# Optimization experiments

Hardware: AMD Instinct MI355X
Metric: run time of the kernel (lower is better)

## Reference

```python
import jax, jax.numpy as jnp
import numpy as np

EPS = 0.1  # FAConv default eps


def setup_inputs() -> dict:
    key = jax.random.key(0)
    k1, k2, k3, k4, k5 = jax.random.split(key, 5)
    N, D, E, Dout = 50000, 128, 600000, 128
    x = jax.random.normal(k1, (N, D), dtype=jnp.float32)
    edge_index = jax.random.randint(k2, (2, E), 0, N, dtype=jnp.int64)
    # glorot-style scale for att vectors (Linear(D,1)) and weight matrix
    att_l = jax.random.normal(k3, (D,), dtype=jnp.float32) * (1.0 / np.sqrt(D))
    att_r = jax.random.normal(k4, (D,), dtype=jnp.float32) * (1.0 / np.sqrt(D))
    weight = jax.random.normal(k5, (D, Dout), dtype=jnp.float32) * np.sqrt(6.0 / (D + Dout))
    bias = jnp.zeros((Dout,), dtype=jnp.float32)
    return {"x": x, "edge_index": edge_index, "att_l": att_l, "att_r": att_r,
            "weight": weight, "bias": bias}


def reference(x, edge_index, att_l, att_r, weight, bias):
    N, D = x.shape
    # gcn_norm with add_self_loops=True
    loops = jnp.arange(N, dtype=edge_index.dtype)
    row = jnp.concatenate([edge_index[0], loops])  # source nodes
    col = jnp.concatenate([edge_index[1], loops])  # target nodes
    deg = jax.ops.segment_sum(jnp.ones_like(col, dtype=x.dtype), col, num_segments=N)
    dinv = jnp.where(deg > 0, jax.lax.rsqrt(jnp.maximum(deg, 1e-12)), 0.0)
    norm = dinv[row] * dinv[col]  # [E+N]
    # FAConv attention: alpha = tanh(att_l . x_j + att_r . x_i)
    al = x @ att_l  # [N]
    ar = x @ att_r  # [N]
    a = jnp.tanh(al[row] + ar[col])  # per-edge
    msg = x[row] * (a * norm)[:, None]  # [E+N, D]
    agg = jax.ops.segment_sum(msg, col, num_segments=N)
    h = agg + EPS * x  # x_0 == x in SAGNN.forward
    return h @ weight + bias
```

## Files before the change

kernel.cpp:

```cpp
#include <hip/hip_runtime.h>
#include <hip/hip_bf16.h>

#define FA_EPS 0.1f
#define BUCKET_M 48

typedef _Float16 half8  __attribute__((ext_vector_type(8)));
typedef _Float16 half4v __attribute__((ext_vector_type(4)));
typedef float    f32x4  __attribute__((ext_vector_type(4)));

__device__ __forceinline__ float fast_tanh(float x) {
    float z = __builtin_amdgcn_exp2f(x * 2.885390081777927f);
    return 1.f - 2.f * __builtin_amdgcn_rcpf(z + 1.f);
}


__global__ __launch_bounds__(256) void k_node_prep(
    const float* __restrict__ x,
    const float* __restrict__ att_l,
    const float* __restrict__ att_r,
    const float* __restrict__ w,
    uint2* __restrict__ R, float* __restrict__ ar,
    _Float16* __restrict__ x16, _Float16* __restrict__ wt, int N)
{
    int gtid = (int)(blockIdx.x * blockDim.x + threadIdx.x);
    if (gtid < 128 * 128) {
        int k = gtid >> 7, n = gtid & 127;
        wt[n * 128 + k] = (_Float16)w[k * 128 + n];
    }
    int wave = gtid >> 6;
    int lane = threadIdx.x & 63;
    int half = lane >> 5;
    int sl   = lane & 31;
    int node = wave * 2 + half;
    if (node >= N) return;
    const float4* xr = (const float4*)(x + (size_t)node * 128);
    float4 v  = xr[sl];
    float4 l4 = ((const float4*)att_l)[sl];
    float4 r4 = ((const float4*)att_r)[sl];
    half4v hv;
    hv[0] = (_Float16)v.x; hv[1] = (_Float16)v.y;
    hv[2] = (_Float16)v.z; hv[3] = (_Float16)v.w;
    *((half4v*)(x16 + (size_t)node * 128) + sl) = hv;
    float pal = v.x * l4.x + v.y * l4.y + v.z * l4.z + v.w * l4.w;
    float par = v.x * r4.x + v.y * r4.y + v.z * r4.z + v.w * r4.w;
    #pragma unroll
    for (int off = 16; off > 0; off >>= 1) {
        pal += __shfl_xor(pal, off);
        par += __shfl_xor(par, off);
    }
    if (sl == 0) {
        R[node] = make_uint2(0u, __float_as_uint(pal));
        ar[node] = par;
    }
}

__global__ __launch_bounds__(256) void k_edge(
    const int* __restrict__ ei,
    uint2* __restrict__ R,
    unsigned int* __restrict__ csr, int E)
{
    int e = (int)(blockIdx.x * blockDim.x + threadIdx.x);
    if (e >= E) return;
    int s = ei[e];
    int t = ei[E + e];
    unsigned int pos = atomicAdd((unsigned int*)(R + t), 1u);
    if (pos < BUCKET_M)
        csr[(size_t)t * BUCKET_M + pos] = (unsigned int)s;
}

__global__ __launch_bounds__(256) void k_gather(
    const _Float16* __restrict__ x16,
    const unsigned int* __restrict__ csr,
    const uint2* __restrict__ R,
    const float* __restrict__ ar,
    _Float16* __restrict__ h16, int N)
{
    int wave = (int)((blockIdx.x * blockDim.x + threadIdx.x) >> 6);
    int lane = threadIdx.x & 63;
    int g  = lane >> 4;
    int sl = lane & 15;
    int t  = wave * 4 + g;
    bool valid = t < N;
    int tc = valid ? t : N - 1;
    uint2 rt = R[tc];
    unsigned int dt = rt.x;
    float al_t = __uint_as_float(rt.y);
    float ar_t = ar[tc];
    unsigned int cnt = dt < BUCKET_M ? dt : BUCKET_M;
    if (!valid) cnt = 0u;
    float dinv_t = __builtin_amdgcn_rsqf((float)(dt + 1u));
    const unsigned int* cs = csr + (size_t)tc * BUCKET_M;
    float acc[8];
    #pragma unroll
    for (int c = 0; c < 8; ++c) acc[c] = 0.f;
    int gbase = lane & 0x30;
    for (unsigned int j0 = 0; j0 < cnt; j0 += 16) {
        unsigned int nb = cnt - j0; if (nb > 16u) nb = 16u;
        unsigned int myidx = j0 + (unsigned int)sl;
        bool own = myidx < cnt;
        unsigned int em = cs[own ? myidx : cnt - 1u];
        uint2 rsm = R[em];
        float am = own ? fast_tanh(__uint_as_float(rsm.y) + ar_t)
                         * __builtin_amdgcn_rsqf((float)(rsm.x + 1u))
                       : 0.f;
        const uint4* bp = (const uint4*)(cs + j0);
        uint4 b0 = bp[0], b1 = bp[1], b2 = bp[2], b3 = bp[3];
        unsigned int eu[16];
        eu[0]=b0.x;  eu[1]=b0.y;  eu[2]=b0.z;  eu[3]=b0.w;
        eu[4]=b1.x;  eu[5]=b1.y;  eu[6]=b1.z;  eu[7]=b1.w;
        eu[8]=b2.x;  eu[9]=b2.y;  eu[10]=b2.z; eu[11]=b2.w;
        eu[12]=b3.x; eu[13]=b3.y; eu[14]=b3.z; eu[15]=b3.w;
        half8 v[16];
        #pragma unroll
        for (int u = 0; u < 16; ++u) {
            unsigned int e = (u < (int)nb) ? eu[u] : 0u;
            v[u] = *((const half8*)(x16 + (size_t)e * 128) + sl);
        }
        #pragma unroll
        for (int u = 0; u < 16; ++u) {
            float a = __shfl(am, gbase + u);
            #pragma unroll
            for (int c = 0; c < 8; ++c) acc[c] += a * (float)v[u][c];
        }
    }
    float selfc = fast_tanh(al_t + ar_t) * dinv_t * dinv_t + FA_EPS;
    half8 vt = *((const half8*)(x16 + (size_t)tc * 128) + sl);
    #pragma unroll
    for (int c = 0; c < 8; ++c) acc[c] = acc[c] * dinv_t + selfc * (float)vt[c];
    if (valid) {
        half8 hv;
        #pragma unroll
        for (int c = 0; c < 8; ++c) hv[c] = (_Float16)acc[c];
        *((half8*)(h16 + (size_t)t * 128) + sl) = hv;
    }
}

__global__ __launch_bounds__(256) void k_matmul_mfma(
    const _Float16* __restrict__ h16,
    const _Float16* __restrict__ wt,
    const float* __restrict__ bias,
    float* __restrict__ out, int N)
{
    __shared__ _Float16 wl[128 * 136];
    int tid = threadIdx.x;
    {
        const float* wsrc = (const float*)wt;
        float* wdst = (float*)wl;
        #pragma unroll
        for (int i = tid; i < 8192; i += 256)
            wdst[(i >> 6) * 68 + (i & 63)] = wsrc[i];
    }
    __syncthreads();
    int wv   = tid >> 6;
    int lane = tid & 63;
    int m    = lane & 15;
    int quad = lane >> 4;
    int r0 = (int)blockIdx.x * 64 + wv * 16;
    f32x4 acc[8];
    #pragma unroll
    for (int t = 0; t < 8; ++t) acc[t] = (f32x4)0.f;
    const _Float16* arow = h16 + (size_t)(r0 + m) * 128 + quad * 8;
    #pragma unroll
    for (int k0 = 0; k0 < 128; k0 += 32) {
        half8 a = *(const half8*)(arow + k0);
        #pragma unroll
        for (int t = 0; t < 8; ++t) {
            const _Float16* bp = wl + (size_t)(t * 16 + m) * 136 + quad * 8 + k0;
            half8 b = *(const half8*)bp;
            acc[t] = __builtin_amdgcn_mfma_f32_16x16x32_f16(a, b, acc[t], 0, 0, 0);
        }
    }
    int orow = r0 + quad * 4;
    #pragma unroll
    for (int t = 0; t < 8; ++t) {
        int col = t * 16 + m;
        float bc = bias[col];
        #pragma unroll
        for (int rg = 0; rg < 4; ++rg) {
            int r = orow + rg;
            if (r < N) out[(size_t)r * 128 + col] = acc[t][rg] + bc;
        }
    }
}

extern "C" void kernel_launch(void* const* d_in, const int* in_sizes, int n_in,
                              void* d_out, int out_size, void* d_ws, size_t ws_size,
                              hipStream_t stream)
{
    const float* x     = (const float*)d_in[0];
    const int*   ei    = (const int*)d_in[1];
    const float* att_l = (const float*)d_in[2];
    const float* att_r = (const float*)d_in[3];
    const float* w     = (const float*)d_in[4];
    const float* bias  = (const float*)d_in[5];
    float* out = (float*)d_out;

    const int N  = in_sizes[0] / 128;
    const int E  = in_sizes[1] / 2;
    const int NP = ((N + 63) / 64) * 64;

    char* ws = (char*)d_ws;
    _Float16*     h16 = (_Float16*)ws;
    _Float16*     x16 = h16 + (size_t)NP * 128;
    uint2*        R   = (uint2*)(x16 + (size_t)N * 128);
    float*        ar  = (float*)(R + N);
    unsigned int* csr = (unsigned int*)(ar + N);
    _Float16*     wt  = (_Float16*)(csr + (size_t)N * BUCKET_M);

    {
        int waves = (N + 1) / 2;
        k_node_prep<<<(waves * 64 + 255) / 256, 256, 0, stream>>>(
            x, att_l, att_r, w, R, ar, x16, wt, N);
    }
    k_edge<<<(E + 255) / 256, 256, 0, stream>>>(ei, R, csr, E);
    {
        int waves = (N + 3) / 4;
        k_gather<<<(waves * 64 + 255) / 256, 256, 0, stream>>>(
            x16, csr, R, ar, h16, N);
    }
    k_matmul_mfma<<<NP / 64, 256, 0, stream>>>(h16, wt, bias, out, N);
}
```

Before: 156.6 us.

## Fuse neighbor gather into MFMA matmul via shared-memory staging of h

Merges the gather/aggregation kernel and the MFMA matmul kernel into one. Each block aggregates 64 target rows into an LDS tile, then multiplies that tile by the LDS-resident weight. This removes the fp16 h round trip through global memory and one kernel launch. In exchange it uses more LDS per block and has fewer independent waves per row chunk, which may lower occupancy and the latency hiding of the random gathers.

```diff
diff --git a/kernel.cpp b/kernel.cpp
--- a/kernel.cpp
+++ b/kernel.cpp
@@ -68,80 +68,17 @@
         csr[(size_t)t * BUCKET_M + pos] = (unsigned int)s;
 }
 
-__global__ __launch_bounds__(256) void k_gather(
+__global__ __launch_bounds__(256) void k_gather_mm(
     const _Float16* __restrict__ x16,
     const unsigned int* __restrict__ csr,
     const uint2* __restrict__ R,
     const float* __restrict__ ar,
-    _Float16* __restrict__ h16, int N)
-{
-    int wave = (int)((blockIdx.x * blockDim.x + threadIdx.x) >> 6);
-    int lane = threadIdx.x & 63;
-    int g  = lane >> 4;
-    int sl = lane & 15;
-    int t  = wave * 4 + g;
-    bool valid = t < N;
-    int tc = valid ? t : N - 1;
-    uint2 rt = R[tc];
-    unsigned int dt = rt.x;
-    float al_t = __uint_as_float(rt.y);
-    float ar_t = ar[tc];
-    unsigned int cnt = dt < BUCKET_M ? dt : BUCKET_M;
-    if (!valid) cnt = 0u;
-    float dinv_t = __builtin_amdgcn_rsqf((float)(dt + 1u));
-    const unsigned int* cs = csr + (size_t)tc * BUCKET_M;
-    float acc[8];
-    #pragma unroll
-    for (int c = 0; c < 8; ++c) acc[c] = 0.f;
-    int gbase = lane & 0x30;
-    for (unsigned int j0 = 0; j0 < cnt; j0 += 16) {
-        unsigned int nb = cnt - j0; if (nb > 16u) nb = 16u;
-        unsigned int myidx = j0 + (unsigned int)sl;
-        bool own = myidx < cnt;
-        unsigned int em = cs[own ? myidx : cnt - 1u];
-        uint2 rsm = R[em];
-        float am = own ? fast_tanh(__uint_as_float(rsm.y) + ar_t)
-                         * __builtin_amdgcn_rsqf((float)(rsm.x + 1u))
-                       : 0.f;
-        const uint4* bp = (const uint4*)(cs + j0);
-        uint4 b0 = bp[0], b1 = bp[1], b2 = bp[2], b3 = bp[3];
-        unsigned int eu[16];
-        eu[0]=b0.x;  eu[1]=b0.y;  eu[2]=b0.z;  eu[3]=b0.w;
-        eu[4]=b1.x;  eu[5]=b1.y;  eu[6]=b1.z;  eu[7]=b1.w;
-        eu[8]=b2.x;  eu[9]=b2.y;  eu[10]=b2.z; eu[11]=b2.w;
-        eu[12]=b3.x; eu[13]=b3.y; eu[14]=b3.z; eu[15]=b3.w;
-        half8 v[16];
-        #pragma unroll
-        for (int u = 0; u < 16; ++u) {
-            unsigned int e = (u < (int)nb) ? eu[u] : 0u;
-            v[u] = *((const half8*)(x16 + (size_t)e * 128) + sl);
-        }
-        #pragma unroll
-        for (int u = 0; u < 16; ++u) {
-            float a = __shfl(am, gbase + u);
-            #pragma unroll
-            for (int c = 0; c < 8; ++c) acc[c] += a * (float)v[u][c];
-        }
-    }
-    float selfc = fast_tanh(al_t + ar_t) * dinv_t * dinv_t + FA_EPS;
-    half8 vt = *((const half8*)(x16 + (size_t)tc * 128) + sl);
-    #pragma unroll
-    for (int c = 0; c < 8; ++c) acc[c] = acc[c] * dinv_t + selfc * (float)vt[c];
-    if (valid) {
-        half8 hv;
-        #pragma unroll
-        for (int c = 0; c < 8; ++c) hv[c] = (_Float16)acc[c];
-        *((half8*)(h16 + (size_t)t * 128) + sl) = hv;
-    }
-}
-
-__global__ __launch_bounds__(256) void k_matmul_mfma(
-    const _Float16* __restrict__ h16,
     const _Float16* __restrict__ wt,
     const float* __restrict__ bias,
     float* __restrict__ out, int N)
 {
     __shared__ _Float16 wl[128 * 136];
+    __shared__ _Float16 hl[64 * 136];
     int tid = threadIdx.x;
     {
         const float* wsrc = (const float*)wt;
@@ -150,16 +87,71 @@
         for (int i = tid; i < 8192; i += 256)
             wdst[(i >> 6) * 68 + (i & 63)] = wsrc[i];
     }
+    int wv    = tid >> 6;
+    int lane  = tid & 63;
+    int g     = lane >> 4;
+    int sl    = lane & 15;
+    int gbase = lane & 0x30;
+
+    for (int sub = 0; sub < 4; ++sub) {
+        int row = wv * 16 + sub * 4 + g;
+        int t   = (int)blockIdx.x * 64 + row;
+        int tc  = t < N ? t : N - 1;
+        uint2 rt = R[tc];
+        unsigned int dt = rt.x;
+        float al_t = __uint_as_float(rt.y);
+        float ar_t = ar[tc];
+        unsigned int cnt = dt < BUCKET_M ? dt : BUCKET_M;
+        float dinv_t = __builtin_amdgcn_rsqf((float)(dt + 1u));
+        const unsigned int* cs = csr + (size_t)tc * BUCKET_M;
+        float acc[8];
+        #pragma unroll
+        for (int c = 0; c < 8; ++c) acc[c] = 0.f;
+        for (unsigned int j0 = 0; j0 < cnt; j0 += 16) {
+            unsigned int nb = cnt - j0; if (nb > 16u) nb = 16u;
+            unsigned int myidx = j0 + (unsigned int)sl;
+            bool own = myidx < cnt;
+            unsigned int em = cs[own ? myidx : cnt - 1u];
+            uint2 rsm = R[em];
+            float am = own ? fast_tanh(__uint_as_float(rsm.y) + ar_t)
+                             * __builtin_amdgcn_rsqf((float)(rsm.x + 1u))
+                           : 0.f;
+            const uint4* bp = (const uint4*)(cs + j0);
+            uint4 b0 = bp[0], b1 = bp[1], b2 = bp[2], b3 = bp[3];
+            unsigned int eu[16];
+            eu[0]=b0.x;  eu[1]=b0.y;  eu[2]=b0.z;  eu[3]=b0.w;
+            eu[4]=b1.x;  eu[5]=b1.y;  eu[6]=b1.z;  eu[7]=b1.w;
+            eu[8]=b2.x;  eu[9]=b2.y;  eu[10]=b2.z; eu[11]=b2.w;
+            eu[12]=b3.x; eu[13]=b3.y; eu[14]=b3.z; eu[15]=b3.w;
+            half8 v[16];
+            #pragma unroll
+            for (int u = 0; u < 16; ++u) {
+                unsigned int e = (u < (int)nb) ? eu[u] : 0u;
+                v[u] = *((const half8*)(x16 + (size_t)e * 128) + sl);
+            }
+            #pragma unroll
+            for (int u = 0; u < 16; ++u) {
+                float a = __shfl(am, gbase + u);
+                #pragma unroll
+                for (int c = 0; c < 8; ++c) acc[c] += a * (float)v[u][c];
+            }
+        }
+        float selfc = fast_tanh(al_t + ar_t) * dinv_t * dinv_t + FA_EPS;
+        half8 vt = *((const half8*)(x16 + (size_t)tc * 128) + sl);
+        half8 hv;
+        #pragma unroll
+        for (int c = 0; c < 8; ++c)
+            hv[c] = (_Float16)(acc[c] * dinv_t + selfc * (float)vt[c]);
+        *(half8*)(&hl[row * 136 + sl * 8]) = hv;
+    }
     __syncthreads();
-    int wv   = tid >> 6;
-    int lane = tid & 63;
+
     int m    = lane & 15;
     int quad = lane >> 4;
-    int r0 = (int)blockIdx.x * 64 + wv * 16;
     f32x4 acc[8];
     #pragma unroll
     for (int t = 0; t < 8; ++t) acc[t] = (f32x4)0.f;
-    const _Float16* arow = h16 + (size_t)(r0 + m) * 128 + quad * 8;
+    const _Float16* arow = hl + (size_t)(wv * 16 + m) * 136 + quad * 8;
     #pragma unroll
     for (int k0 = 0; k0 < 128; k0 += 32) {
         half8 a = *(const half8*)(arow + k0);
@@ -170,6 +162,7 @@
             acc[t] = __builtin_amdgcn_mfma_f32_16x16x32_f16(a, b, acc[t], 0, 0, 0);
         }
     }
+    int r0   = (int)blockIdx.x * 64 + wv * 16;
     int orow = r0 + quad * 4;
     #pragma unroll
     for (int t = 0; t < 8; ++t) {
@@ -200,8 +193,7 @@
     const int NP = ((N + 63) / 64) * 64;
 
     char* ws = (char*)d_ws;
-    _Float16*     h16 = (_Float16*)ws;
-    _Float16*     x16 = h16 + (size_t)NP * 128;
+    _Float16*     x16 = (_Float16*)ws;
     uint2*        R   = (uint2*)(x16 + (size_t)N * 128);
     float*        ar  = (float*)(R + N);
     unsigned int* csr = (unsigned int*)(ar + N);
@@ -213,10 +205,6 @@
             x, att_l, att_r, w, R, ar, x16, wt, N);
     }
     k_edge<<<(E + 255) / 256, 256, 0, stream>>>(ei, R, csr, E);
-    {
-        int waves = (N + 3) / 4;
-        k_gather<<<(waves * 64 + 255) / 256, 256, 0, stream>>>(
-            x16, csr, R, ar, h16, N);
-    }
-    k_matmul_mfma<<<NP / 64, 256, 0, stream>>>(h16, wt, bias, out, N);
-}
+    k_gather_mm<<<NP / 64, 256, 0, stream>>>(
+        x16, csr, R, ar, wt, bias, out, N);
+}
```

Measured after the change: 166.7 us. 1.06x slower.
